# Kernel tuning notes

Measured on AMD Instinct MI355X. Metric: run time of the kernel, lower is better.

## Reference

```python
import jax, jax.numpy as jnp
import numpy as np

DIV_VAL = 11.313708498984761  # sqrt(128), the softmax temperature used as div_val


def setup_inputs() -> dict:
    key = jax.random.key(0)
    kq, kk, kv = jax.random.split(key, 3)
    B, Lq, Lk, D = 16, 4096, 4096, 128
    return {
        "query": jax.random.normal(kq, (B, Lq, D), dtype=jnp.float32),
        "key": jax.random.normal(kk, (B, Lk, D), dtype=jnp.float32),
        "value": jax.random.normal(kv, (B, Lk, D), dtype=jnp.float32),
    }


def reference(query, key, value):
    # qk = Q @ K^T, scaled by 1/div_val  -> [B, Lq, Lk]
    scaled_qk = jnp.einsum("bqd,bkd->bqk", query, key) / DIV_VAL
    # numerically stable softmax over last axis; dropout is identity (eval / p=0)
    attn = jax.nn.softmax(scaled_qk, axis=-1)
    # output = attn @ V -> [B, Lq, Dv]
    return jnp.einsum("bqk,bkd->bqd", attn, value)
```

## Files before the change

### kernel.cpp

```cpp
#include <hip/hip_runtime.h>

#define B_  16
#define L_  4096
#define D_  128
#define NT  (L_ / 64)

typedef __attribute__((ext_vector_type(8)))  __bf16 bf16x8;
typedef __attribute__((ext_vector_type(2)))  __bf16 bf16x2;
typedef __attribute__((ext_vector_type(16))) float  f32x16;
typedef __attribute__((ext_vector_type(4)))  float  f32x4;
typedef __attribute__((ext_vector_type(4)))  int    i32x4;
typedef __attribute__((ext_vector_type(8)))  unsigned short u16x8;
typedef __attribute__((ext_vector_type(4)))  unsigned short u16x4;

#ifndef __has_builtin
#define __has_builtin(x) 0
#endif
#if __has_builtin(__builtin_amdgcn_permlane32_swap)
#define HAVE_PLSWAP 1
#else
#define HAVE_PLSWAP 0
#endif

__device__ __forceinline__ unsigned short f2bf(float f){
  unsigned u = __builtin_bit_cast(unsigned, f);
  u += 0x7fffu + ((u >> 16) & 1u);
  return (unsigned short)(u >> 16);
}

__device__ __forceinline__ int packbf(float a, float b){
  bf16x2 t; t[0] = (__bf16)a; t[1] = (__bf16)b;
  return __builtin_bit_cast(int, t);
}

__device__ __forceinline__ void gload16(const void* g, void* l){
  __builtin_amdgcn_global_load_lds(
      (const __attribute__((address_space(1))) unsigned int*)g,
      (__attribute__((address_space(3))) unsigned int*)l, 16, 0, 0);
}

__device__ __forceinline__ f32x16 z16(){
  f32x16 t;
#pragma unroll
  for (int i = 0; i < 16; ++i) t[i] = 0.f;
  return t;
}

__global__ void cvt_bf16_kernel(const float* __restrict__ in,
                                unsigned short* __restrict__ out, int n8,
                                float scale){
  int i = blockIdx.x * blockDim.x + threadIdx.x;
  if (i >= n8) return;
  const float4* p = reinterpret_cast<const float4*>(in) + (size_t)i * 2;
  float4 a = p[0], b = p[1];
  u16x8 o;
  o[0]=f2bf(a.x*scale); o[1]=f2bf(a.y*scale); o[2]=f2bf(a.z*scale); o[3]=f2bf(a.w*scale);
  o[4]=f2bf(b.x*scale); o[5]=f2bf(b.y*scale); o[6]=f2bf(b.z*scale); o[7]=f2bf(b.w*scale);
  reinterpret_cast<u16x8*>(out)[i] = o;
}

__global__ void transpose_v_kernel(const float* __restrict__ V,
                                   unsigned short* __restrict__ Vt){
  __shared__ unsigned short tile[64][65];
  const int k0 = blockIdx.x * 64, d0 = blockIdx.y * 64, b = blockIdx.z;
  const int tr = threadIdx.x >> 4, tc = threadIdx.x & 15;
  const float* src = V + ((size_t)b * L_ + k0) * D_ + d0;
#pragma unroll
  for (int p = 0; p < 4; ++p){
    int kl = p * 16 + tr;
    float4 v = *reinterpret_cast<const float4*>(src + (size_t)kl * D_ + tc * 4);
    tile[kl][tc*4+0] = f2bf(v.x);
    tile[kl][tc*4+1] = f2bf(v.y);
    tile[kl][tc*4+2] = f2bf(v.z);
    tile[kl][tc*4+3] = f2bf(v.w);
  }
  __syncthreads();
  unsigned short* dst = Vt + (size_t)b * D_ * L_ + (size_t)d0 * L_ + k0;
#pragma unroll
  for (int p = 0; p < 4; ++p){
    int dl = p * 16 + tr;
    u16x4 o;
    o[0] = tile[tc*4+0][dl];
    o[1] = tile[tc*4+1][dl];
    o[2] = tile[tc*4+2][dl];
    o[3] = tile[tc*4+3][dl];
    *reinterpret_cast<u16x4*>(dst + (size_t)dl * L_ + tc * 4) = o;
  }
}

__device__ __forceinline__ bf16x8 mkchunk(float a0,float a1,float a2,float a3,
                                          float a4,float a5,float a6,float a7,
                                          int hi){
  int x0 = packbf(a0,a1), x1 = packbf(a2,a3);
  int x2 = packbf(a4,a5), x3 = packbf(a6,a7);
  int W0, W1, W2, W3;
#if HAVE_PLSWAP
  {
    auto r = __builtin_amdgcn_permlane32_swap((unsigned)x0, (unsigned)x2, false, false);
    W0 = (int)r[0]; W2 = (int)r[1];
  }
  {
    auto r = __builtin_amdgcn_permlane32_swap((unsigned)x1, (unsigned)x3, false, false);
    W1 = (int)r[0]; W3 = (int)r[1];
  }
  (void)hi;
#else
  int y0 = __shfl_xor(x0, 32), y1 = __shfl_xor(x1, 32);
  int y2 = __shfl_xor(x2, 32), y3 = __shfl_xor(x3, 32);
  W0 = hi ? y2 : x0;  W1 = hi ? y3 : x1;
  W2 = hi ? x2 : y0;  W3 = hi ? x3 : y1;
#endif
  i32x4 ww; ww[0]=W0; ww[1]=W1; ww[2]=W2; ww[3]=W3;
  return __builtin_bit_cast(bf16x8, ww);
}

__global__ __launch_bounds__(512, 1)
void attn_kernel(const float* __restrict__ Q,
                 const unsigned short* __restrict__ Kb,
                 const unsigned short* __restrict__ Vt,
                 float* __restrict__ out){
  __shared__ char smem[131072];
  char* Klds = smem;
  char* Vlds = smem + 65536;

  const int tid = threadIdx.x;
  const int w = tid >> 6, l = tid & 63;
  const int row = l & 31, hi = l >> 5;
  const int swz = (row & 15) << 4;
  const int b = blockIdx.x, qt = blockIdx.y;

  const float* qptr = Q + ((size_t)b * L_ + (size_t)qt * 256 + w * 32 + row) * D_;
  bf16x8 qf[8];
#pragma unroll
  for (int c = 0; c < 8; ++c){
    float4 a  = *reinterpret_cast<const float4*>(qptr + c * 16 + hi * 8);
    float4 bb = *reinterpret_cast<const float4*>(qptr + c * 16 + hi * 8 + 4);
    u16x8 o;
    o[0]=f2bf(a.x);  o[1]=f2bf(a.y);  o[2]=f2bf(a.z);  o[3]=f2bf(a.w);
    o[4]=f2bf(bb.x); o[5]=f2bf(bb.y); o[6]=f2bf(bb.z); o[7]=f2bf(bb.w);
    qf[c] = __builtin_bit_cast(bf16x8, o);
  }

  const char* Kg = (const char*)(Kb + (size_t)b * L_ * D_);
  const char* Vg = (const char*)(Vt + (size_t)b * (size_t)D_ * L_);

  f32x16 o[4];
#pragma unroll
  for (int n = 0; n < 4; ++n) o[n] = z16();
  const f32x16 ZERO = z16();
  float ln = 0.f;

  auto STAGE = [&](int bsel, int t){
    char* kd = Klds + bsel * 16384;
    char* vd = Vlds + bsel * 16384;
    const int kv0 = t * 64;
#pragma unroll
    for (int j = 0; j < 2; ++j){
      int idx = j * 512 + tid;
      int kr = idx >> 4, sc = idx & 15;
      int clog = (sc << 4) ^ ((kr & 15) << 4);
      gload16(Kg + (size_t)(kv0 + kr) * 256 + clog, kd + idx * 16);
    }
#pragma unroll
    for (int j = 0; j < 2; ++j){
      int idx = j * 512 + tid;
      int lr = idx >> 4, sc = idx & 15;
      int clog = (sc << 4) ^ ((lr & 15) << 4);
      int dd = lr + ((clog >> 7) << 6);
      gload16(Vg + (size_t)dd * (L_ * 2) + (size_t)kv0 * 2 + (clog & 127),
              vd + idx * 16);
    }
  };

#define SMC(P, J)                                                              \
      P[(J)+0] = __builtin_amdgcn_exp2f(P[(J)+0]);                             \
      P[(J)+1] = __builtin_amdgcn_exp2f(P[(J)+1]);                             \
      P[(J)+2] = __builtin_amdgcn_exp2f(P[(J)+2]);                             \
      P[(J)+3] = __builtin_amdgcn_exp2f(P[(J)+3]);                             \
      ln += (P[(J)+0] + P[(J)+1]) + (P[(J)+2] + P[(J)+3]);

#define KF2(KC, C)                                                             \
      bf16x8 kf0 = *(const bf16x8*)((KC) + row * 256 + (((C)*32 + hi*16) ^ swz)); \
      bf16x8 kf1 = *(const bf16x8*)((KC) + (row+32) * 256 + (((C)*32 + hi*16) ^ swz));

#define PVG(VP, G, PA)                                                         \
    {                                                                          \
      bf16x8 v0 = *(const bf16x8*)((VP) + (0*32 + row) * 256 + (((G)*32 + hi*16) ^ swz));          \
      bf16x8 v1 = *(const bf16x8*)((VP) + (1*32 + row) * 256 + (((G)*32 + hi*16) ^ swz));          \
      bf16x8 v2 = *(const bf16x8*)((VP) + (0*32 + row) * 256 + ((128 + (G)*32 + hi*16) ^ swz));    \
      bf16x8 v3 = *(const bf16x8*)((VP) + (1*32 + row) * 256 + ((128 + (G)*32 + hi*16) ^ swz));    \
      o[0] = __builtin_amdgcn_mfma_f32_32x32x16_bf16(v0, PA, o[0], 0, 0, 0);   \
      o[1] = __builtin_amdgcn_mfma_f32_32x32x16_bf16(v1, PA, o[1], 0, 0, 0);   \
      o[2] = __builtin_amdgcn_mfma_f32_32x32x16_bf16(v2, PA, o[2], 0, 0, 0);   \
      o[3] = __builtin_amdgcn_mfma_f32_32x32x16_bf16(v3, PA, o[3], 0, 0, 0);   \
    }

#define PVALL(VP, P0, P1)                                                      \
    bf16x8 pa0 = mkchunk(P0[0],P0[1],P0[2],P0[3],P0[4],P0[5],P0[6],P0[7], hi); \
    bf16x8 pa1 = mkchunk(P0[8],P0[9],P0[10],P0[11],P0[12],P0[13],P0[14],P0[15], hi); \
    PVG(Vp_, 0, pa0)                                                           \
    bf16x8 pa2 = mkchunk(P1[0],P1[1],P1[2],P1[3],P1[4],P1[5],P1[6],P1[7], hi); \
    PVG(Vp_, 1, pa1)                                                           \
    bf16x8 pa3 = mkchunk(P1[8],P1[9],P1[10],P1[11],P1[12],P1[13],P1[14],P1[15], hi); \
    PVG(Vp_, 2, pa2)                                                           \
    PVG(Vp_, 3, pa3)

#define BODY(I, C0, C1, P0, P1)                                                \
  {                                                                            \
    const int i_ = (I);                                                        \
    if (i_ + 2 < NT) STAGE((i_ + 2) & 3, i_ + 2);                              \
    const char* Kc_ = Klds + (i_ & 3) * 16384;                                 \
    const char* Vp_ = Vlds + ((i_ - 1) & 3) * 16384;                           \
    __builtin_amdgcn_s_setprio(1);                                             \
    {                                      \
      KF2(Kc_, 0)                                                              \
      C0 = __builtin_amdgcn_mfma_f32_32x32x16_bf16(kf0, qf[0], ZERO, 0, 0, 0); \
      C1 = __builtin_amdgcn_mfma_f32_32x32x16_bf16(kf1, qf[0], ZERO, 0, 0, 0); \
      SMC(P0, 0)                                                               \
    }                                                                          \
    _Pragma("unroll")                                                          \
    for (int c = 1; c < 8; ++c){                                               \
      KF2(Kc_, c)                                                              \
      C0 = __builtin_amdgcn_mfma_f32_32x32x16_bf16(kf0, qf[c], C0, 0, 0, 0);   \
      C1 = __builtin_amdgcn_mfma_f32_32x32x16_bf16(kf1, qf[c], C1, 0, 0, 0);   \
      if (c < 4) { SMC(P0, 4*c) } else { SMC(P1, 4*(c-4)) }                    \
    }                                                                          \
    PVALL(Vp_, P0, P1)                                                         \
    __builtin_amdgcn_s_setprio(0);                                             \
    if (i_ + 2 < NT) { asm volatile("s_waitcnt vmcnt(4)" ::: "memory"); }      \
    else             { asm volatile("s_waitcnt vmcnt(0)" ::: "memory"); }      \
    __builtin_amdgcn_s_barrier();                                              \
  }

  STAGE(0, 0); STAGE(1, 1); STAGE(2, 2);
  asm volatile("s_waitcnt vmcnt(4)" ::: "memory");
  __builtin_amdgcn_s_barrier();

  f32x16 sA0, sA1, sB0, sB1;
  {
    const char* Kc_ = Klds;
    __builtin_amdgcn_s_setprio(1);
    {
      KF2(Kc_, 0)
      sA0 = __builtin_amdgcn_mfma_f32_32x32x16_bf16(kf0, qf[0], ZERO, 0, 0, 0);
      sA1 = __builtin_amdgcn_mfma_f32_32x32x16_bf16(kf1, qf[0], ZERO, 0, 0, 0);
    }
#pragma unroll
    for (int c = 1; c < 8; ++c){
      KF2(Kc_, c)
      sA0 = __builtin_amdgcn_mfma_f32_32x32x16_bf16(kf0, qf[c], sA0, 0, 0, 0);
      sA1 = __builtin_amdgcn_mfma_f32_32x32x16_bf16(kf1, qf[c], sA1, 0, 0, 0);
    }
    __builtin_amdgcn_s_setprio(0);
  }

  for (int i = 1; i <= NT - 3; i += 2){
    BODY(i,     sB0, sB1, sA0, sA1);
    BODY(i + 1, sA0, sA1, sB0, sB1);
  }
  BODY(NT - 1, sB0, sB1, sA0, sA1);
  {
    const char* Vp_ = Vlds + ((NT - 1) & 3) * 16384;
#pragma unroll
    for (int j = 0; j < 16; j += 4) { SMC(sB0, j) }
#pragma unroll
    for (int j = 0; j < 16; j += 4) { SMC(sB1, j) }
    __builtin_amdgcn_s_setprio(1);
    PVALL(Vp_, sB0, sB1)
    __builtin_amdgcn_s_setprio(0);
  }

  float lt = ln + __shfl_xor(ln, 32);
  float inv = 1.0f / lt;
  float* outp = out + ((size_t)b * L_ + (size_t)qt * 256 + w * 32 + row) * D_;
#pragma unroll
  for (int n = 0; n < 4; ++n)
#pragma unroll
    for (int rq = 0; rq < 4; ++rq){
      f32x4 v4;
      v4[0] = o[n][rq*4+0] * inv;
      v4[1] = o[n][rq*4+1] * inv;
      v4[2] = o[n][rq*4+2] * inv;
      v4[3] = o[n][rq*4+3] * inv;
      *reinterpret_cast<f32x4*>(outp + n * 32 + rq * 8 + hi * 4) = v4;
    }
}

extern "C" void kernel_launch(void* const* d_in, const int* in_sizes, int n_in,
                              void* d_out, int out_size, void* d_ws, size_t ws_size,
                              hipStream_t stream){
  const float* Q = (const float*)d_in[0];
  const float* K = (const float*)d_in[1];
  const float* V = (const float*)d_in[2];
  float* out = (float*)d_out;

  const size_t NE = (size_t)B_ * L_ * D_;
  unsigned short* kb = (unsigned short*)d_ws;
  unsigned short* vt = kb + NE;

  const float SCALE_L2E = 1.4426950408889634f / 11.313708498984761f;
  int n8 = (int)(NE / 8);
  cvt_bf16_kernel<<<dim3(n8 / 256), 256, 0, stream>>>(K, kb, n8, SCALE_L2E);
  transpose_v_kernel<<<dim3(L_ / 64, D_ / 64, B_), 256, 0, stream>>>(V, vt);
  attn_kernel<<<dim3(B_, L_ / 256), 512, 0, stream>>>(Q, kb, vt, out);
}
```

Measured before the change: 168.9 us.

## Read K fragments directly from global memory instead of staging through LDS

K tiles are no longer copied into shared memory. Each wave now loads its K MFMA operands straight from global memory, and only V keeps the asynchronous LDS pipeline, with the wait count and the V staging point adjusted to match. The aim is to cut LDS traffic and the LDS write/read cost for K, but it puts global-load latency directly in front of the QK MFMAs with no prefetch. A waves-per-EU attribute is also added.

```diff
diff --git a/kernel.cpp b/kernel.cpp
--- a/kernel.cpp
+++ b/kernel.cpp
@@ -114,14 +114,13 @@
   return __builtin_bit_cast(bf16x8, ww);
 }
 
-__global__ __launch_bounds__(512, 1)
+__global__ __launch_bounds__(512, 1) __attribute__((amdgpu_waves_per_eu(1, 2)))
 void attn_kernel(const float* __restrict__ Q,
                  const unsigned short* __restrict__ Kb,
                  const unsigned short* __restrict__ Vt,
                  float* __restrict__ out){
   __shared__ char smem[131072];
-  char* Klds = smem;
-  char* Vlds = smem + 65536;
+  char* Vlds = smem;
 
   const int tid = threadIdx.x;
   const int w = tid >> 6, l = tid & 63;
@@ -151,16 +150,8 @@
   float ln = 0.f;
 
   auto STAGE = [&](int bsel, int t){
-    char* kd = Klds + bsel * 16384;
     char* vd = Vlds + bsel * 16384;
     const int kv0 = t * 64;
-#pragma unroll
-    for (int j = 0; j < 2; ++j){
-      int idx = j * 512 + tid;
-      int kr = idx >> 4, sc = idx & 15;
-      int clog = (sc << 4) ^ ((kr & 15) << 4);
-      gload16(Kg + (size_t)(kv0 + kr) * 256 + clog, kd + idx * 16);
-    }
 #pragma unroll
     for (int j = 0; j < 2; ++j){
       int idx = j * 512 + tid;
@@ -179,9 +170,9 @@
       P[(J)+3] = __builtin_amdgcn_exp2f(P[(J)+3]);                             \
       ln += (P[(J)+0] + P[(J)+1]) + (P[(J)+2] + P[(J)+3]);
 
-#define KF2(KC, C)                                                             \
-      bf16x8 kf0 = *(const bf16x8*)((KC) + row * 256 + (((C)*32 + hi*16) ^ swz)); \
-      bf16x8 kf1 = *(const bf16x8*)((KC) + (row+32) * 256 + (((C)*32 + hi*16) ^ swz));
+#define KF2G(KP, C)                                                            \
+      bf16x8 kf0 = *(const bf16x8*)((KP) + (C)*32);                            \
+      bf16x8 kf1 = *(const bf16x8*)((KP) + 32*256 + (C)*32);
 
 #define PVG(VP, G, PA)                                                         \
     {                                                                          \
@@ -208,46 +199,46 @@
 #define BODY(I, C0, C1, P0, P1)                                                \
   {                                                                            \
     const int i_ = (I);                                                        \
-    if (i_ + 2 < NT) STAGE((i_ + 2) & 3, i_ + 2);                              \
-    const char* Kc_ = Klds + (i_ & 3) * 16384;                                 \
+    const char* Kp_ = Kg + ((size_t)i_ * 64 + row) * 256 + hi * 16;            \
     const char* Vp_ = Vlds + ((i_ - 1) & 3) * 16384;                           \
     __builtin_amdgcn_s_setprio(1);                                             \
     {                                      \
-      KF2(Kc_, 0)                                                              \
+      KF2G(Kp_, 0)                                                             \
       C0 = __builtin_amdgcn_mfma_f32_32x32x16_bf16(kf0, qf[0], ZERO, 0, 0, 0); \
       C1 = __builtin_amdgcn_mfma_f32_32x32x16_bf16(kf1, qf[0], ZERO, 0, 0, 0); \
       SMC(P0, 0)                                                               \
     }                                                                          \
     _Pragma("unroll")                                                          \
     for (int c = 1; c < 8; ++c){                                               \
-      KF2(Kc_, c)                                                              \
+      KF2G(Kp_, c)                                                             \
       C0 = __builtin_amdgcn_mfma_f32_32x32x16_bf16(kf0, qf[c], C0, 0, 0, 0);   \
       C1 = __builtin_amdgcn_mfma_f32_32x32x16_bf16(kf1, qf[c], C1, 0, 0, 0);   \
       if (c < 4) { SMC(P0, 4*c) } else { SMC(P1, 4*(c-4)) }                    \
     }                                                                          \
     PVALL(Vp_, P0, P1)                                                         \
     __builtin_amdgcn_s_setprio(0);                                             \
-    if (i_ + 2 < NT) { asm volatile("s_waitcnt vmcnt(4)" ::: "memory"); }      \
+    if (i_ + 2 < NT) { STAGE((i_ + 2) & 3, i_ + 2);                            \
+                       asm volatile("s_waitcnt vmcnt(2)" ::: "memory"); }      \
     else             { asm volatile("s_waitcnt vmcnt(0)" ::: "memory"); }      \
     __builtin_amdgcn_s_barrier();                                              \
   }
 
   STAGE(0, 0); STAGE(1, 1); STAGE(2, 2);
-  asm volatile("s_waitcnt vmcnt(4)" ::: "memory");
+  asm volatile("s_waitcnt vmcnt(0)" ::: "memory");
   __builtin_amdgcn_s_barrier();
 
   f32x16 sA0, sA1, sB0, sB1;
   {
-    const char* Kc_ = Klds;
+    const char* Kp_ = Kg + (size_t)row * 256 + hi * 16;
     __builtin_amdgcn_s_setprio(1);
     {
-      KF2(Kc_, 0)
+      KF2G(Kp_, 0)
       sA0 = __builtin_amdgcn_mfma_f32_32x32x16_bf16(kf0, qf[0], ZERO, 0, 0, 0);
       sA1 = __builtin_amdgcn_mfma_f32_32x32x16_bf16(kf1, qf[0], ZERO, 0, 0, 0);
     }
 #pragma unroll
     for (int c = 1; c < 8; ++c){
-      KF2(Kc_, c)
+      KF2G(Kp_, c)
       sA0 = __builtin_amdgcn_mfma_f32_32x32x16_bf16(kf0, qf[c], sA0, 0, 0, 0);
       sA1 = __builtin_amdgcn_mfma_f32_32x32x16_bf16(kf1, qf[c], sA1, 0, 0, 0);
     }
```

Result: slower. 345.6 us (+104.6%).
